# Kernel tuning notes

Measured on AMD Instinct MI355X. Metric: run time of the kernel, lower is better.

The kernel has to match this reference:

```python
import jax, jax.numpy as jnp
import numpy as np

K = 8          # number of nearest neighbors (init kwarg k)
CONST = 0.1    # inverseweight const
NUM = 1.0      # inverseweight num


def setup_inputs() -> dict:
    key = jax.random.key(0)
    k1, k2 = jax.random.split(key)
    data1 = jax.random.normal(k1, (4096, 1024), dtype=jnp.float32)
    data2 = jax.random.normal(k2, (8192, 1024), dtype=jnp.float32)
    return {"data1": data1, "data2": data2}


def reference(data1, data2):
    # pairwise Euclidean distance (torch.dist with p=2): [N, M]
    x2 = jnp.sum(data1 * data1, axis=1, keepdims=True)          # [N, 1]
    y2 = jnp.sum(data2 * data2, axis=1)                         # [M]
    d2 = x2 + y2[None, :] - 2.0 * (data1 @ data2.T)             # [N, M]
    dist = jnp.sqrt(jnp.maximum(d2, 1e-12))

    # k smallest distances and their indices
    neg_top, idx = jax.lax.top_k(-dist, K)                      # [N, K]
    knn_dist = -neg_top                                         # [N, K]

    # inverse weighting: w = num / (dist + const)
    w = NUM / (knn_dist + CONST)                                # [N, K]

    # gather neighbor vectors and weighted-average them
    neigh = data2[idx]                                          # [N, K, D]
    out = jnp.einsum('nk,nkd->nd', w, neigh) / jnp.sum(w, axis=1, keepdims=True)
    return out
```

## Files before the change

### kernel.cpp

```cpp
#include <hip/hip_runtime.h>


typedef short bf16x8 __attribute__((ext_vector_type(8)));
typedef float f32x4 __attribute__((ext_vector_type(4)));

#define SENTINEL 1e30f
#define BKK 32

static __device__ __forceinline__ unsigned short f2bf(float f) {
  unsigned u = __float_as_uint(f);
  return (unsigned short)((u + 0x7fffu + ((u >> 16) & 1u)) >> 16);
}

__global__ __launch_bounds__(256) void convert_all_kernel(
    const float* __restrict__ A, const float* __restrict__ B,
    unsigned short* __restrict__ Abf, unsigned short* __restrict__ Bbf,
    float* __restrict__ y2, int N) {
  const int bid = blockIdx.x;
  const int tid = threadIdx.x;
  if (bid < N) {
    const float4 v = ((const float4*)&A[(size_t)bid * 1024])[tid];
    ushort4 o;
    o.x = f2bf(v.x); o.y = f2bf(v.y); o.z = f2bf(v.z); o.w = f2bf(v.w);
    ((ushort4*)&Abf[(size_t)bid * 1024])[tid] = o;
  } else {
    const int m = bid - N;
    __shared__ float red[256];
    const float4 v = ((const float4*)&B[(size_t)m * 1024])[tid];
    ushort4 o;
    o.x = f2bf(v.x); o.y = f2bf(v.y); o.z = f2bf(v.z); o.w = f2bf(v.w);
    ((ushort4*)&Bbf[(size_t)m * 1024])[tid] = o;
    red[tid] = v.x * v.x + v.y * v.y + v.z * v.z + v.w * v.w;
    __syncthreads();
    for (int s = 128; s > 0; s >>= 1) {
      if (tid < s) red[tid] += red[tid + s];
      __syncthreads();
    }
    if (tid == 0) y2[m] = red[0];
  }
}

#define CAS(sa, ia, sb, ib)                         \
  do {                                              \
    if ((sa) > (sb)) {                              \
      const float _t = (sa); (sa) = (sb); (sb) = _t;\
      const int _u = (ia); (ia) = (ib); (ib) = _u;  \
    }                                               \
  } while (0)

#define STAGE(sk, b)                                                          \
  do {                                                                        \
    const unsigned short* gA_ =                                               \
        Abf + (size_t)(r0 + w * 32 + srow) * 1024 + (sk) * 32 + sofs;         \
    const unsigned short* gB_ =                                               \
        Bbf + (size_t)(c0 + w * 64 + srow) * 1024 + (sk) * 32 + sofs;         \
    __builtin_amdgcn_global_load_lds(                                         \
        (const __attribute__((address_space(1))) void*)gA_,                   \
        (__attribute__((address_space(3))) void*)&As[b][(w * 32) * 32],       \
        16, 0, 0);                                                            \
    __builtin_amdgcn_global_load_lds(                                         \
        (const __attribute__((address_space(1))) void*)(gA_ + (size_t)16 * 1024), \
        (__attribute__((address_space(3))) void*)&As[b][(w * 32 + 16) * 32],  \
        16, 0, 0);                                                            \
    _Pragma("unroll")                                                         \
    for (int l_ = 0; l_ < 4; ++l_)                                            \
      __builtin_amdgcn_global_load_lds(                                       \
          (const __attribute__((address_space(1))) void*)(gB_ + (size_t)(16 * l_) * 1024), \
          (__attribute__((address_space(3))) void*)&Bs[b][(w * 64 + 16 * l_) * 32], \
          16, 0, 0);                                                          \
  } while (0)

#define COMPUTE(b)                                                            \
  do {                                                                        \
    bf16x8 af[4], bfr[8];                                                     \
    _Pragma("unroll")                                                         \
    for (int fi = 0; fi < 4; ++fi)                                            \
      af[fi] = *(const bf16x8*)&As[b][(frowA + fi * 16) * 32 + fofs];         \
    _Pragma("unroll")                                                         \
    for (int fj = 0; fj < 8; ++fj)                                            \
      bfr[fj] = *(const bf16x8*)&Bs[b][(frowB + fj * 16) * 32 + fofs];        \
    __builtin_amdgcn_s_setprio(1);                                            \
    _Pragma("unroll")                                                         \
    for (int fi = 0; fi < 4; ++fi)                                            \
      _Pragma("unroll")                                                       \
      for (int fj = 0; fj < 8; ++fj)                                          \
        acc[fi][fj] = __builtin_amdgcn_mfma_f32_16x16x32_bf16(                \
            bfr[fj], af[fi], acc[fi][fj], 0, 0, 0);                           \
    __builtin_amdgcn_s_setprio(0);                                            \
  } while (0)

#define PIPE_SYNC(N)                                                          \
  do {                                                                        \
    asm volatile("s_waitcnt vmcnt(" #N ")" ::: "memory");                     \
    __builtin_amdgcn_sched_barrier(0);                                        \
    __builtin_amdgcn_s_barrier();                                             \
    __builtin_amdgcn_sched_barrier(0);                                        \
  } while (0)

__global__ __launch_bounds__(256, 2) void screen6_kernel(
    const unsigned short* __restrict__ Abf, const unsigned short* __restrict__ Bbf,
    const float* __restrict__ y2g,
    float* __restrict__ cand_s, int* __restrict__ cand_i) {
  __shared__ unsigned short As[3][128 * 32];
  __shared__ unsigned short Bs[3][256 * 32];

  const int tid = threadIdx.x;
  const int w = tid >> 6;
  const int lane = tid & 63;
  const int wr = w >> 1, wc = w & 1;

  const int v = blockIdx.x + gridDim.x * blockIdx.y;
  const int bx = (v & 7) * 2 + ((v >> 3) & 1);
  const int by = v >> 4;
  const int r0 = by * 128;

  const int srow = lane >> 2;
  const int sofs = ((lane & 3) ^ ((lane >> 3) & 3)) * 8;

  const int frowA = wr * 64 + (lane & 15);
  const int frowB = wc * 128 + (lane & 15);
  const int fofs = ((lane >> 4) ^ ((lane >> 1) & 3)) * 8;
  const int cgrp = (lane >> 4) * 4;

  for (int chunk = 0; chunk < 2; ++chunk) {
    const int c0 = bx * 512 + chunk * 256;
    __syncthreads();

    f32x4 acc[4][8];
#pragma unroll
    for (int fi = 0; fi < 4; ++fi)
#pragma unroll
      for (int fj = 0; fj < 8; ++fj) {
        f32x4 z = {0.f, 0.f, 0.f, 0.f};
        acc[fi][fj] = z;
      }

    STAGE(0, 0);
    STAGE(1, 1);
    int cA = 0, cB = 1, cC = 2;
    for (int t = 0; t < 31; ++t) {
      PIPE_SYNC(6);
      if (t < 30) STAGE(t + 2, cC);
      __builtin_amdgcn_sched_barrier(0);
      COMPUTE(cA);
      const int tmp = cA; cA = cB; cB = cC; cC = tmp;
    }
    PIPE_SYNC(0);
    COMPUTE(cA);

    float4 y2v[8];
#pragma unroll
    for (int fj = 0; fj < 8; ++fj)
      y2v[fj] = *(const float4*)&y2g[c0 + wc * 128 + fj * 16 + cgrp];

#pragma unroll
    for (int fi = 0; fi < 4; ++fi) {
      float ls[8];
      int li[8];
#pragma unroll
      for (int j = 0; j < 8; ++j) { ls[j] = SENTINEL; li[j] = 0x7fffffff; }
      const int cb = c0 + wc * 128 + cgrp;
#pragma unroll
      for (int fj = 0; fj < 8; ++fj) {
#pragma unroll
        for (int reg = 0; reg < 4; ++reg) {
          const float s = y2v[fj][reg] - 2.0f * acc[fi][fj][reg];
          if (s < ls[7]) {
            ls[7] = s; li[7] = cb + fj * 16 + reg;
#pragma unroll
            for (int j = 7; j > 0; --j) {
              if (ls[j] < ls[j - 1]) {
                const float t = ls[j]; ls[j] = ls[j - 1]; ls[j - 1] = t;
                const int u = li[j]; li[j] = li[j - 1]; li[j - 1] = u;
              }
            }
          }
        }
      }
#pragma unroll
      for (int off = 16; off <= 32; off <<= 1) {
        float rs[8];
        int ri[8];
#pragma unroll
        for (int j = 0; j < 8; ++j) {
          rs[j] = __shfl_xor(ls[j], off, 64);
          ri[j] = __shfl_xor(li[j], off, 64);
        }
        float ms[8];
        int mi_[8];
#pragma unroll
        for (int i = 0; i < 8; ++i) {
          const bool t = ls[i] < rs[7 - i];
          ms[i] = t ? ls[i] : rs[7 - i];
          mi_[i] = t ? li[i] : ri[7 - i];
        }
        CAS(ms[0], mi_[0], ms[4], mi_[4]);
        CAS(ms[1], mi_[1], ms[5], mi_[5]);
        CAS(ms[2], mi_[2], ms[6], mi_[6]);
        CAS(ms[3], mi_[3], ms[7], mi_[7]);
        CAS(ms[0], mi_[0], ms[2], mi_[2]);
        CAS(ms[1], mi_[1], ms[3], mi_[3]);
        CAS(ms[4], mi_[4], ms[6], mi_[6]);
        CAS(ms[5], mi_[5], ms[7], mi_[7]);
        CAS(ms[0], mi_[0], ms[1], mi_[1]);
        CAS(ms[2], mi_[2], ms[3], mi_[3]);
        CAS(ms[4], mi_[4], ms[5], mi_[5]);
        CAS(ms[6], mi_[6], ms[7], mi_[7]);
#pragma unroll
        for (int j = 0; j < 8; ++j) { ls[j] = ms[j]; li[j] = mi_[j]; }
      }
      if ((lane >> 4) == 0) {
        const int row = r0 + wr * 64 + fi * 16 + lane;
        const size_t base =
            ((size_t)row * 64 + wc * 32 + bx * 2 + chunk) * 8;
#pragma unroll
        for (int j = 0; j < 8; ++j) {
          cand_s[base + j] = ls[j];
          cand_i[base + j] = li[j];
        }
      }
    }
  }
}

__global__ __launch_bounds__(256) void finalize5_kernel(
    const float* __restrict__ A, const float* __restrict__ B,
    const float* __restrict__ y2g,
    const float* __restrict__ cand_s, const int* __restrict__ cand_i,
    float* __restrict__ out) {
  const int tid = threadIdx.x;
  const int w = tid >> 6;
  const int lane = tid & 63;
  const int rloc = w >> 1;
  const int wh = w & 1;
  const int n = blockIdx.x * 2 + rloc;
  __shared__ float comb[2][2][16];

  float s12[12];
  int i12[12];
  {
    const float4* cs = (const float4*)&cand_s[(size_t)n * 512 + lane * 8];
    const int4* cj = (const int4*)&cand_i[(size_t)n * 512 + lane * 8];
    const float4 sa = cs[0], sb = cs[1];
    const int4 ja = cj[0], jb = cj[1];
    s12[0] = sa.x; s12[1] = sa.y; s12[2] = sa.z; s12[3] = sa.w;
    s12[4] = sb.x; s12[5] = sb.y; s12[6] = sb.z; s12[7] = sb.w;
    i12[0] = ja.x; i12[1] = ja.y; i12[2] = ja.z; i12[3] = ja.w;
    i12[4] = jb.x; i12[5] = jb.y; i12[6] = jb.z; i12[7] = jb.w;
#pragma unroll
    for (int j = 8; j < 12; ++j) { s12[j] = SENTINEL; i12[j] = 0x7fffffff; }
  }

#pragma unroll
  for (int off = 1; off <= 32; off <<= 1) {
    float rs[12];
    int ri[12];
#pragma unroll
    for (int j = 0; j < 12; ++j) {
      rs[j] = __shfl_xor(s12[j], off, 64);
      ri[j] = __shfl_xor(i12[j], off, 64);
    }
    float ms[12];
    int mj[12];
#pragma unroll
    for (int j = 0; j < 12; ++j) {
      const bool tke = s12[j] < rs[11 - j];
      ms[j] = tke ? s12[j] : rs[11 - j];
      mj[j] = tke ? i12[j] : ri[11 - j];
    }
    CAS(ms[0], mj[0], ms[8], mj[8]);  CAS(ms[1], mj[1], ms[9], mj[9]);
    CAS(ms[2], mj[2], ms[10], mj[10]); CAS(ms[3], mj[3], ms[11], mj[11]);
    CAS(ms[4], mj[4], ms[8], mj[8]);  CAS(ms[5], mj[5], ms[9], mj[9]);
    CAS(ms[6], mj[6], ms[10], mj[10]); CAS(ms[7], mj[7], ms[11], mj[11]);
    CAS(ms[0], mj[0], ms[2], mj[2]);  CAS(ms[1], mj[1], ms[3], mj[3]);
    CAS(ms[4], mj[4], ms[6], mj[6]);  CAS(ms[5], mj[5], ms[7], mj[7]);
    CAS(ms[8], mj[8], ms[10], mj[10]); CAS(ms[9], mj[9], ms[11], mj[11]);
    CAS(ms[0], mj[0], ms[1], mj[1]);  CAS(ms[2], mj[2], ms[3], mj[3]);
    CAS(ms[4], mj[4], ms[5], mj[5]);  CAS(ms[6], mj[6], ms[7], mj[7]);
    CAS(ms[8], mj[8], ms[9], mj[9]);  CAS(ms[10], mj[10], ms[11], mj[11]);
#pragma unroll
    for (int j = 0; j < 12; ++j) { s12[j] = ms[j]; i12[j] = mj[j]; }
  }

  const float4* Arow = (const float4*)&A[(size_t)n * 1024];
  const int fbase = wh * 128 + lane * 2;
  float4 a4[2];
  a4[0] = Arow[fbase];
  a4[1] = Arow[fbase + 1];
  float part[13];
#pragma unroll
  for (int r = 0; r < 13; ++r) part[r] = 0.0f;
  part[12] = a4[0].x * a4[0].x + a4[0].y * a4[0].y + a4[0].z * a4[0].z +
             a4[0].w * a4[0].w + a4[1].x * a4[1].x + a4[1].y * a4[1].y +
             a4[1].z * a4[1].z + a4[1].w * a4[1].w;
#pragma unroll
  for (int p = 0; p < 2; ++p) {
    float4 b[12];
#pragma unroll
    for (int j = 0; j < 12; ++j)
      b[j] = ((const float4*)&B[(size_t)i12[j] * 1024])[fbase + p];
#pragma unroll
    for (int j = 0; j < 12; ++j)
      part[j] += a4[p].x * b[j].x + a4[p].y * b[j].y + a4[p].z * b[j].z +
                 a4[p].w * b[j].w;
  }
#pragma unroll
  for (int r = 0; r < 13; ++r) {
#pragma unroll
    for (int off = 32; off >= 1; off >>= 1) part[r] += __shfl_xor(part[r], off, 64);
  }
  if (lane == 0) {
#pragma unroll
    for (int r = 0; r < 13; ++r) comb[rloc][wh][r] = part[r];
  }
  __syncthreads();
  float tot[13];
#pragma unroll
  for (int r = 0; r < 13; ++r) tot[r] = comb[rloc][0][r] + comb[rloc][1][r];

  const float x2 = tot[12];
  float d2v[12];
  bool used[12];
#pragma unroll
  for (int j = 0; j < 12; ++j) {
    d2v[j] = x2 + y2g[i12[j]] - 2.0f * tot[j];
    used[j] = false;
  }
  float wk[8];
  int wi[8];
  float wsum = 0.0f;
  for (int k = 0; k < 8; ++k) {
    float bd = SENTINEL;
    int bi = 0x7fffffff, bslot = 0;
#pragma unroll
    for (int j = 0; j < 12; ++j) {
      if (used[j]) continue;
      const float d2 = d2v[j];
      if (d2 < bd || (d2 == bd && i12[j] < bi)) { bd = d2; bi = i12[j]; bslot = j; }
    }
    used[bslot] = true;
    const float d2c = fmaxf(bd, 1e-12f);
    const float wv = 1.0f / (sqrtf(d2c) + 0.1f);
    wk[k] = wv; wi[k] = bi; wsum += wv;
  }
  const float inv = 1.0f / wsum;

  float4 o0 = {0, 0, 0, 0}, o1 = {0, 0, 0, 0};
#pragma unroll
  for (int k = 0; k < 8; ++k) {
    const float wv = wk[k];
    const float4* Brow = (const float4*)&B[(size_t)wi[k] * 1024];
    const float4 b0 = Brow[fbase];
    const float4 b1 = Brow[fbase + 1];
    o0.x += wv * b0.x; o0.y += wv * b0.y; o0.z += wv * b0.z; o0.w += wv * b0.w;
    o1.x += wv * b1.x; o1.y += wv * b1.y; o1.z += wv * b1.z; o1.w += wv * b1.w;
  }
  o0.x *= inv; o0.y *= inv; o0.z *= inv; o0.w *= inv;
  o1.x *= inv; o1.y *= inv; o1.z *= inv; o1.w *= inv;
  float4* Orow = (float4*)&out[(size_t)n * 1024];
  Orow[fbase] = o0;
  Orow[fbase + 1] = o1;
}

__global__ __launch_bounds__(256) void rownorm_kernel(
    const float* __restrict__ B, float* __restrict__ y2) {
  const int m = blockIdx.x;
  const int tid = threadIdx.x;
  __shared__ float red[256];
  const float4 v = *(const float4*)&B[(size_t)m * 1024 + tid * 4];
  red[tid] = v.x * v.x + v.y * v.y + v.z * v.z + v.w * v.w;
  __syncthreads();
  for (int s = 128; s > 0; s >>= 1) {
    if (tid < s) red[tid] += red[tid + s];
    __syncthreads();
  }
  if (tid == 0) y2[m] = red[0];
}

__global__ __launch_bounds__(256) void knn_chunk_kernel(
    const float* __restrict__ A, const float* __restrict__ B,
    const float* __restrict__ y2g,
    float* __restrict__ cand_s, int* __restrict__ cand_i) {
  __shared__ float As[BKK][68];
  __shared__ float Bs[BKK][68];
  __shared__ float Sc[64][65];

  const int tid = threadIdx.x;
  const int tx = tid & 15;
  const int ty = tid >> 4;
  const int r0 = blockIdx.y * 64;
  const int c0 = blockIdx.x * 1024;
  const int lrow = tid >> 3;
  const int lk = (tid & 7) * 4;

  float top_s[8];
  int top_i[8];
#pragma unroll
  for (int j = 0; j < 8; ++j) { top_s[j] = SENTINEL; top_i[j] = 0x7fffffff; }

  for (int tile = 0; tile < 16; ++tile) {
    const int cbase = c0 + tile * 64;
    float acc[4][4];
#pragma unroll
    for (int i = 0; i < 4; ++i)
#pragma unroll
      for (int j = 0; j < 4; ++j) acc[i][j] = 0.0f;

    for (int k0 = 0; k0 < 1024; k0 += BKK) {
      const float4 a0 = *(const float4*)&A[(size_t)(r0 + lrow) * 1024 + k0 + lk];
      const float4 a1 = *(const float4*)&A[(size_t)(r0 + lrow + 32) * 1024 + k0 + lk];
      const float4 b0 = *(const float4*)&B[(size_t)(cbase + lrow) * 1024 + k0 + lk];
      const float4 b1 = *(const float4*)&B[(size_t)(cbase + lrow + 32) * 1024 + k0 + lk];
      __syncthreads();
      As[lk + 0][lrow] = a0.x; As[lk + 1][lrow] = a0.y;
      As[lk + 2][lrow] = a0.z; As[lk + 3][lrow] = a0.w;
      As[lk + 0][lrow + 32] = a1.x; As[lk + 1][lrow + 32] = a1.y;
      As[lk + 2][lrow + 32] = a1.z; As[lk + 3][lrow + 32] = a1.w;
      Bs[lk + 0][lrow] = b0.x; Bs[lk + 1][lrow] = b0.y;
      Bs[lk + 2][lrow] = b0.z; Bs[lk + 3][lrow] = b0.w;
      Bs[lk + 0][lrow + 32] = b1.x; Bs[lk + 1][lrow + 32] = b1.y;
      Bs[lk + 2][lrow + 32] = b1.z; Bs[lk + 3][lrow + 32] = b1.w;
      __syncthreads();
#pragma unroll
      for (int kk = 0; kk < BKK; ++kk) {
        const float4 av = *(const float4*)&As[kk][ty * 4];
        const float4 bv = *(const float4*)&Bs[kk][tx * 4];
        acc[0][0] += av.x * bv.x; acc[0][1] += av.x * bv.y;
        acc[0][2] += av.x * bv.z; acc[0][3] += av.x * bv.w;
        acc[1][0] += av.y * bv.x; acc[1][1] += av.y * bv.y;
        acc[1][2] += av.y * bv.z; acc[1][3] += av.y * bv.w;
        acc[2][0] += av.z * bv.x; acc[2][1] += av.z * bv.y;
        acc[2][2] += av.z * bv.z; acc[2][3] += av.z * bv.w;
        acc[3][0] += av.w * bv.x; acc[3][1] += av.w * bv.y;
        acc[3][2] += av.w * bv.z; acc[3][3] += av.w * bv.w;
      }
    }
#pragma unroll
    for (int i = 0; i < 4; ++i) {
      const int row = ty * 4 + i;
#pragma unroll
      for (int j = 0; j < 4; ++j) {
        const int col = tx * 4 + j;
        Sc[row][col] = y2g[cbase + col] - 2.0f * acc[i][j];
      }
    }
    __syncthreads();
    if (tid < 64) {
      for (int c = 0; c < 64; ++c) {
        const float s = Sc[tid][c];
        if (s < top_s[7]) {
          top_s[7] = s; top_i[7] = cbase + c;
#pragma unroll
          for (int j = 7; j > 0; --j) {
            if (top_s[j] < top_s[j - 1]) {
              const float tss = top_s[j]; top_s[j] = top_s[j - 1]; top_s[j - 1] = tss;
              const int tii = top_i[j]; top_i[j] = top_i[j - 1]; top_i[j - 1] = tii;
            }
          }
        }
      }
    }
  }

  if (tid < 64) {
    const int n = r0 + tid;
    const int base = (n * gridDim.x + blockIdx.x) * 8;
#pragma unroll
    for (int j = 0; j < 8; ++j) {
      cand_s[base + j] = top_s[j];
      cand_i[base + j] = top_i[j];
    }
  }
}

__global__ __launch_bounds__(256) void finalize_kernel(
    const float* __restrict__ A, const float* __restrict__ B,
    const float* __restrict__ cand_s, const int* __restrict__ cand_i,
    float* __restrict__ out, int nchunks) {
  const int n = blockIdx.x;
  const int tid = threadIdx.x;
  __shared__ float red[256];
  __shared__ float ls[64];
  __shared__ int li[64];
  __shared__ float wsh2[8];
  __shared__ int wid[8];
  __shared__ float wsum_sh;

  const int ncand = nchunks * 8;
  const float4 a = *(const float4*)&A[(size_t)n * 1024 + tid * 4];
  red[tid] = a.x * a.x + a.y * a.y + a.z * a.z + a.w * a.w;
  if (tid < ncand) {
    ls[tid] = cand_s[n * ncand + tid];
    li[tid] = cand_i[n * ncand + tid];
  }
  __syncthreads();
  for (int s = 128; s > 0; s >>= 1) {
    if (tid < s) red[tid] += red[tid + s];
    __syncthreads();
  }
  if (tid == 0) {
    const float x2 = red[0];
    float wsum = 0.0f;
    for (int j = 0; j < 8; ++j) {
      float bs = SENTINEL;
      int bi = 0x7fffffff;
      int bp = 0;
      for (int c = 0; c < ncand; ++c) {
        const float s_ = ls[c];
        const int i_ = li[c];
        if (s_ < bs || (s_ == bs && i_ < bi)) { bs = s_; bi = i_; bp = c; }
      }
      ls[bp] = SENTINEL; li[bp] = 0x7fffffff;
      float d2 = x2 + bs;
      d2 = fmaxf(d2, 1e-12f);
      const float wkk = 1.0f / (sqrtf(d2) + 0.1f);
      wsh2[j] = wkk; wid[j] = bi;
      wsum += wkk;
    }
    wsum_sh = wsum;
  }
  __syncthreads();
  const float inv = 1.0f / wsum_sh;
  float ox = 0.0f, oy = 0.0f, oz = 0.0f, ow = 0.0f;
#pragma unroll
  for (int j = 0; j < 8; ++j) {
    const float wkk = wsh2[j];
    const float4 v = *(const float4*)&B[(size_t)wid[j] * 1024 + tid * 4];
    ox += wkk * v.x; oy += wkk * v.y; oz += wkk * v.z; ow += wkk * v.w;
  }
  float4 o;
  o.x = ox * inv; o.y = oy * inv; o.z = oz * inv; o.w = ow * inv;
  *(float4*)&out[(size_t)n * 1024 + tid * 4] = o;
}

extern "C" void kernel_launch(void* const* d_in, const int* in_sizes, int n_in,
                              void* d_out, int out_size, void* d_ws, size_t ws_size,
                              hipStream_t stream) {
  const float* A = (const float*)d_in[0];
  const float* Bm = (const float*)d_in[1];
  const int D = 1024;
  const int N = in_sizes[0] / D;
  const int M = in_sizes[1] / D;

  const size_t needA = (size_t)N * D * 2;
  const size_t needB = (size_t)M * D * 2;
  const size_t needC = (size_t)N * 512 * 4;
  const size_t need = needA + needB + (size_t)M * 4 + 2 * needC;

  if (ws_size >= need && M == 8192 && N % 128 == 0 && N % 2 == 0) {
    unsigned short* Abf = (unsigned short*)d_ws;
    unsigned short* Bbf = Abf + (size_t)N * D;
    float* y2 = (float*)(Bbf + (size_t)M * D);
    float* cand_s = y2 + M;
    int* cand_i = (int*)(cand_s + (size_t)N * 512);

    convert_all_kernel<<<N + M, 256, 0, stream>>>(A, Bm, Abf, Bbf, y2, N);
    dim3 g(M / 512, N / 128);
    screen6_kernel<<<g, 256, 0, stream>>>(Abf, Bbf, y2, cand_s, cand_i);
    finalize5_kernel<<<N / 2, 256, 0, stream>>>(A, Bm, y2, cand_s, cand_i,
                                                (float*)d_out);
  } else {
    float* y2 = (float*)d_ws;
    float* cand_s = y2 + M;
    int* cand_i = (int*)(cand_s + (size_t)N * 64);
    rownorm_kernel<<<M, 256, 0, stream>>>(Bm, y2);
    dim3 gridB(M / 1024, N / 64);
    knn_chunk_kernel<<<gridB, 256, 0, stream>>>(A, Bm, y2, cand_s, cand_i);
    finalize_kernel<<<N, 256, 0, stream>>>(A, Bm, cand_s, cand_i, (float*)d_out, M / 1024);
  }
}
```

Baseline: 335.4 us.

## Split screen kernel across eight waves with smaller per-wave tiles

The GEMM screening kernel now launches 512 threads (8 waves) per 128x256 tile instead of 256, so each wave owns 32 rows instead of 64. This halves the accumulator registers per wave and the per-wave staging loads, and the launch bound asks for 4 blocks per CU. The y2 - 2*acc epilogue is folded into the accumulators up front, so the separate y2 vector array is no longer kept live. The trade-off is that more waves share the same LDS tile, so B fragments are re-read from LDS twice as often relative to MFMA work.

```diff
diff --git a/kernel.cpp b/kernel.cpp
--- a/kernel.cpp
+++ b/kernel.cpp
@@ -51,37 +51,35 @@
 #define STAGE(sk, b)                                                          \
   do {                                                                        \
     const unsigned short* gA_ =                                               \
-        Abf + (size_t)(r0 + w * 32 + srow) * 1024 + (sk) * 32 + sofs;         \
+        Abf + (size_t)(r0 + w * 16 + srow) * 1024 + (sk) * 32 + sofs;         \
     const unsigned short* gB_ =                                               \
-        Bbf + (size_t)(c0 + w * 64 + srow) * 1024 + (sk) * 32 + sofs;         \
+        Bbf + (size_t)(c0 + w * 32 + srow) * 1024 + (sk) * 32 + sofs;         \
     __builtin_amdgcn_global_load_lds(                                         \
         (const __attribute__((address_space(1))) void*)gA_,                   \
-        (__attribute__((address_space(3))) void*)&As[b][(w * 32) * 32],       \
+        (__attribute__((address_space(3))) void*)&As[b][(w * 16) * 32],       \
         16, 0, 0);                                                            \
     __builtin_amdgcn_global_load_lds(                                         \
-        (const __attribute__((address_space(1))) void*)(gA_ + (size_t)16 * 1024), \
-        (__attribute__((address_space(3))) void*)&As[b][(w * 32 + 16) * 32],  \
+        (const __attribute__((address_space(1))) void*)gB_,                   \
+        (__attribute__((address_space(3))) void*)&Bs[b][(w * 32) * 32],       \
         16, 0, 0);                                                            \
-    _Pragma("unroll")                                                         \
-    for (int l_ = 0; l_ < 4; ++l_)                                            \
-      __builtin_amdgcn_global_load_lds(                                       \
-          (const __attribute__((address_space(1))) void*)(gB_ + (size_t)(16 * l_) * 1024), \
-          (__attribute__((address_space(3))) void*)&Bs[b][(w * 64 + 16 * l_) * 32], \
-          16, 0, 0);                                                          \
+    __builtin_amdgcn_global_load_lds(                                         \
+        (const __attribute__((address_space(1))) void*)(gB_ + (size_t)16 * 1024), \
+        (__attribute__((address_space(3))) void*)&Bs[b][(w * 32 + 16) * 32],  \
+        16, 0, 0);                                                            \
   } while (0)
 
 #define COMPUTE(b)                                                            \
   do {                                                                        \
-    bf16x8 af[4], bfr[8];                                                     \
+    bf16x8 af[2], bfr[8];                                                     \
     _Pragma("unroll")                                                         \
-    for (int fi = 0; fi < 4; ++fi)                                            \
+    for (int fi = 0; fi < 2; ++fi)                                            \
       af[fi] = *(const bf16x8*)&As[b][(frowA + fi * 16) * 32 + fofs];         \
     _Pragma("unroll")                                                         \
     for (int fj = 0; fj < 8; ++fj)                                            \
       bfr[fj] = *(const bf16x8*)&Bs[b][(frowB + fj * 16) * 32 + fofs];        \
     __builtin_amdgcn_s_setprio(1);                                            \
     _Pragma("unroll")                                                         \
-    for (int fi = 0; fi < 4; ++fi)                                            \
+    for (int fi = 0; fi < 2; ++fi)                                            \
       _Pragma("unroll")                                                       \
       for (int fj = 0; fj < 8; ++fj)                                          \
         acc[fi][fj] = __builtin_amdgcn_mfma_f32_16x16x32_bf16(                \
@@ -97,7 +95,7 @@
     __builtin_amdgcn_sched_barrier(0);                                        \
   } while (0)
 
-__global__ __launch_bounds__(256, 2) void screen6_kernel(
+__global__ __launch_bounds__(512, 4) void screen7_kernel(
     const unsigned short* __restrict__ Abf, const unsigned short* __restrict__ Bbf,
     const float* __restrict__ y2g,
     float* __restrict__ cand_s, int* __restrict__ cand_i) {
@@ -107,7 +105,8 @@
   const int tid = threadIdx.x;
   const int w = tid >> 6;
   const int lane = tid & 63;
-  const int wr = w >> 1, wc = w & 1;
+  const int wr = w >> 1;
+  const int wc = w & 1;
 
   const int v = blockIdx.x + gridDim.x * blockIdx.y;
   const int bx = (v & 7) * 2 + ((v >> 3) & 1);
@@ -117,7 +116,7 @@
   const int srow = lane >> 2;
   const int sofs = ((lane & 3) ^ ((lane >> 3) & 3)) * 8;
 
-  const int frowA = wr * 64 + (lane & 15);
+  const int frowA = wr * 32 + (lane & 15);
   const int frowB = wc * 128 + (lane & 15);
   const int fofs = ((lane >> 4) ^ ((lane >> 1) & 3)) * 8;
   const int cgrp = (lane >> 4) * 4;
@@ -126,9 +125,9 @@
     const int c0 = bx * 512 + chunk * 256;
     __syncthreads();
 
-    f32x4 acc[4][8];
-#pragma unroll
-    for (int fi = 0; fi < 4; ++fi)
+    f32x4 acc[2][8];
+#pragma unroll
+    for (int fi = 0; fi < 2; ++fi)
 #pragma unroll
       for (int fj = 0; fj < 8; ++fj) {
         f32x4 z = {0.f, 0.f, 0.f, 0.f};
@@ -139,7 +138,7 @@
     STAGE(1, 1);
     int cA = 0, cB = 1, cC = 2;
     for (int t = 0; t < 31; ++t) {
-      PIPE_SYNC(6);
+      PIPE_SYNC(3);
       if (t < 30) STAGE(t + 2, cC);
       __builtin_amdgcn_sched_barrier(0);
       COMPUTE(cA);
@@ -148,13 +147,18 @@
     PIPE_SYNC(0);
     COMPUTE(cA);
 
-    float4 y2v[8];
-#pragma unroll
-    for (int fj = 0; fj < 8; ++fj)
-      y2v[fj] = *(const float4*)&y2g[c0 + wc * 128 + fj * 16 + cgrp];
-
-#pragma unroll
-    for (int fi = 0; fi < 4; ++fi) {
+#pragma unroll
+    for (int fj = 0; fj < 8; ++fj) {
+      const float4 y2q = *(const float4*)&y2g[c0 + wc * 128 + fj * 16 + cgrp];
+#pragma unroll
+      for (int fi = 0; fi < 2; ++fi)
+#pragma unroll
+        for (int reg = 0; reg < 4; ++reg)
+          acc[fi][fj][reg] = y2q[reg] - 2.0f * acc[fi][fj][reg];
+    }
+
+#pragma unroll
+    for (int fi = 0; fi < 2; ++fi) {
       float ls[8];
       int li[8];
 #pragma unroll
@@ -164,7 +168,7 @@
       for (int fj = 0; fj < 8; ++fj) {
 #pragma unroll
         for (int reg = 0; reg < 4; ++reg) {
-          const float s = y2v[fj][reg] - 2.0f * acc[fi][fj][reg];
+          const float s = acc[fi][fj][reg];
           if (s < ls[7]) {
             ls[7] = s; li[7] = cb + fj * 16 + reg;
 #pragma unroll
@@ -210,7 +214,7 @@
         for (int j = 0; j < 8; ++j) { ls[j] = ms[j]; li[j] = mi_[j]; }
       }
       if ((lane >> 4) == 0) {
-        const int row = r0 + wr * 64 + fi * 16 + lane;
+        const int row = r0 + wr * 32 + fi * 16 + lane;
         const size_t base =
             ((size_t)row * 64 + wc * 32 + bx * 2 + chunk) * 8;
 #pragma unroll
@@ -556,7 +560,7 @@
 
     convert_all_kernel<<<N + M, 256, 0, stream>>>(A, Bm, Abf, Bbf, y2, N);
     dim3 g(M / 512, N / 128);
-    screen6_kernel<<<g, 256, 0, stream>>>(Abf, Bbf, y2, cand_s, cand_i);
+    screen7_kernel<<<g, 512, 0, stream>>>(Abf, Bbf, y2, cand_s, cand_i);
     finalize5_kernel<<<N / 2, 256, 0, stream>>>(A, Bm, y2, cand_s, cand_i,
                                                 (float*)d_out);
   } else {
```

Result: no change. 332.1 us (-1.0%).
